# Performance work log

Hardware: AMD Instinct MI355X
Metric: run time of the kernel (lower is better)

The kernel has to match this reference:

```python
import jax, jax.numpy as jnp
import numpy as np
import math

EMBED = 768
HEADS = 12
DK = EMBED // HEADS
FFN = 3072
NQ = 8
B, S = 4, 2048


def _layernorm(x, g, b, eps=1e-5):
    mu = jnp.mean(x, axis=-1, keepdims=True)
    var = jnp.var(x, axis=-1, keepdims=True)
    return (x - mu) * jax.lax.rsqrt(var + eps) * g + b


def setup_inputs() -> dict:
    key = jax.random.key(0)
    ks = jax.random.split(key, 16)
    std = 0.02
    inp = {
        "x": jax.random.normal(ks[0], (B, S, EMBED), dtype=jnp.float32),
        "mask": jnp.ones((B, S), dtype=jnp.int32),
        # attention projections (torch Linear: W [out, in])
        "wq": jax.random.normal(ks[1], (EMBED, EMBED), jnp.float32) * std,
        "bq": jnp.zeros((EMBED,), jnp.float32),
        "wk": jax.random.normal(ks[2], (EMBED, EMBED), jnp.float32) * std,
        "bk": jnp.zeros((EMBED,), jnp.float32),
        "wv": jax.random.normal(ks[3], (EMBED, EMBED), jnp.float32) * std,
        "bv": jnp.zeros((EMBED,), jnp.float32),
        "wo": jax.random.normal(ks[4], (EMBED, EMBED), jnp.float32) * std,
        "bo": jnp.zeros((EMBED,), jnp.float32),
        # layernorms
        "g1": jnp.ones((EMBED,), jnp.float32),
        "be1": jnp.zeros((EMBED,), jnp.float32),
        "g2": jnp.ones((EMBED,), jnp.float32),
        "be2": jnp.zeros((EMBED,), jnp.float32),
        # quantum FFN: trainable RY angles + two linears
        "theta": jax.random.normal(ks[5], (NQ,), jnp.float32) * 0.1,
        "w1": jax.random.normal(ks[6], (FFN, NQ), jnp.float32) * std,
        "b1": jnp.zeros((FFN,), jnp.float32),
        "w2": jax.random.normal(ks[7], (EMBED, FFN), jnp.float32) * std,
        "b2": jnp.zeros((EMBED,), jnp.float32),
    }
    return inp


def _block(x, mask, wq, bq, wk, bk, wv, bv, wo, bo, g1, be1, g2, be2,
           theta, w1, b1, w2, b2):
    b, s, _ = x.shape
    # --- multi-head attention (dropout = identity at eval) ---
    q = (x @ wq.T + bq).reshape(b, s, HEADS, DK)
    k = (x @ wk.T + bk).reshape(b, s, HEADS, DK)
    v = (x @ wv.T + bv).reshape(b, s, HEADS, DK)
    scores = jnp.einsum("bqhd,bkhd->bhqk", q, k) / math.sqrt(DK)
    scores = jnp.where(mask[:, None, None, :] == 0, -1e9, scores)
    attn = jax.nn.softmax(scores, axis=-1)
    ctx = jnp.einsum("bhqk,bkhd->bqhd", attn, v).reshape(b, s, EMBED)
    attn_out = ctx @ wo.T + bo
    x = _layernorm(x + attn_out, g1, be1)
    # --- quantum FFN: RY(x_i) then RY(theta_i) on |0>, <Z> = cos(x_i+theta_i)
    # (product state, no entanglement -> exact closed form, fully batched)
    meas = jnp.cos(x[..., :NQ] + theta)            # [b, s, NQ]
    h = jax.nn.relu(meas @ w1.T + b1)              # [b, s, FFN]
    ffn_out = h @ w2.T + b2                        # [b, s, EMBED]
    return _layernorm(x + ffn_out, g2, be2)


def reference(x, mask, wq, bq, wk, bk, wv, bv, wo, bo, g1, be1, g2, be2,
              theta, w1, b1, w2, b2):
    return _block(x, mask, wq, bq, wk, bk, wv, bv, wo, bo,
                  g1, be1, g2, be2, theta, w1, b1, w2, b2)
```

## Files before the change

### kernel.cpp

```cpp
#include <hip/hip_runtime.h>
#include <hip/hip_bf16.h>


typedef __bf16 bf16_t;
typedef bf16_t bf16x4 __attribute__((ext_vector_type(4)));
typedef bf16_t bf16x8 __attribute__((ext_vector_type(8)));
typedef float floatx4 __attribute__((ext_vector_type(4)));

#define LOG2E 1.44269504088896f

__device__ __forceinline__ void gload16(const bf16_t* g, bf16_t* l) {
    __builtin_amdgcn_global_load_lds(
        (const __attribute__((address_space(1))) unsigned int*)g,
        (__attribute__((address_space(3))) unsigned int*)l,
        16, 0, 0);
}

__global__ __launch_bounds__(256)
void prep(const float* __restrict__ x,
          const float* __restrict__ wq, const float* __restrict__ wk,
          const float* __restrict__ wv, const float* __restrict__ wo,
          const float* __restrict__ w2,
          const float* __restrict__ bq, const float* __restrict__ bk,
          const float* __restrict__ bv,
          bf16_t* __restrict__ xb, bf16_t* __restrict__ wqkv,
          bf16_t* __restrict__ wob, bf16_t* __restrict__ w2b,
          float* __restrict__ bqkv)
{
    const int seg = blockIdx.y;
    const int idx = blockIdx.x * 256 + threadIdx.x;
    if (seg == 0) {
        if (idx >= 1572864) return;
        const float4 f = ((const float4*)x)[idx];
        bf16x4 o = {(bf16_t)f.x, (bf16_t)f.y, (bf16_t)f.z, (bf16_t)f.w};
        ((bf16x4*)xb)[idx] = o;
    } else if (seg == 1) {
        if (idx >= 442368) return;
        const int e = idx * 4;
        float4 f = (e < 589824) ? ((const float4*)wq)[idx]
                 : (e < 1179648) ? ((const float4*)wk)[idx - 147456]
                                 : ((const float4*)wv)[idx - 294912];
        if (e < 589824) { f.x *= 0.125f; f.y *= 0.125f; f.z *= 0.125f; f.w *= 0.125f; }
        bf16x4 o = {(bf16_t)f.x, (bf16_t)f.y, (bf16_t)f.z, (bf16_t)f.w};
        ((bf16x4*)wqkv)[idx] = o;
    } else if (seg == 2) {
        if (idx >= 147456) return;
        const float4 f = ((const float4*)wo)[idx];
        bf16x4 o = {(bf16_t)f.x, (bf16_t)f.y, (bf16_t)f.z, (bf16_t)f.w};
        ((bf16x4*)wob)[idx] = o;
    } else if (seg == 3) {
        if (idx >= 589824) return;
        const float4 f = ((const float4*)w2)[idx];
        bf16x4 o = {(bf16_t)f.x, (bf16_t)f.y, (bf16_t)f.z, (bf16_t)f.w};
        ((bf16x4*)w2b)[idx] = o;
    } else {
        if (idx >= 576) return;
        const int e = idx * 4;
        float4 f = (e < 768) ? ((const float4*)bq)[idx]
                 : (e < 1536) ? ((const float4*)bk)[idx - 192]
                              : ((const float4*)bv)[idx - 384];
        if (e < 768) { f.x *= 0.125f; f.y *= 0.125f; f.z *= 0.125f; f.w *= 0.125f; }
        ((float4*)bqkv)[idx] = f;
    }
}

template<typename TC>
__global__ __launch_bounds__(256)
void gemm_bb(const bf16_t* __restrict__ A, const bf16_t* __restrict__ W,
             const float* __restrict__ bias, TC* __restrict__ C,
             int kPer, int lda, int ldw, int ldc, int splitStride)
{
    __shared__ __align__(16) bf16_t As[2][4096];
    __shared__ __align__(16) bf16_t Bs[2][4096];
    const int tid  = threadIdx.x;
    const int wave = tid >> 6;
    const int lane = tid & 63;
    const int wm = (wave >> 1) * 64;
    const int wn = (wave & 1) * 64;

    const int nwg  = gridDim.x * gridDim.y;
    const int flat = blockIdx.y * gridDim.x + blockIdx.x;
    const int swz  = (flat & 7) * (nwg >> 3) + (flat >> 3);
    const int bm = (swz / gridDim.x) * 128;
    const int bn = (swz % gridDim.x) * 128;

    const int fr = lane & 15;
    const int fk = (lane >> 4) * 8;

    const int kBeg = blockIdx.z * kPer;
    const int kEnd = kBeg + kPer;
    C += (size_t)blockIdx.z * splitStride;

    const int srow = tid >> 2;
    const int scol = (tid & 3) * 8;

    floatx4 acc[4][4] = {};

    const bf16_t* gA = A + (size_t)(bm + srow) * lda + scol;
    const bf16_t* gB = W + (size_t)(bn + srow) * ldw + scol;

#define STAGE(buf, kk)                                              \
    {   const bf16_t* ga = gA + (kk);                               \
        const bf16_t* gb = gB + (kk);                               \
        gload16(ga,                    &As[buf][tid * 8]);          \
        gload16(ga + (size_t)64 * lda, &As[buf][tid * 8 + 2048]);   \
        gload16(gb,                    &Bs[buf][tid * 8]);          \
        gload16(gb + (size_t)64 * ldw, &Bs[buf][tid * 8 + 2048]);   \
    }

    STAGE(0, kBeg);
    __syncthreads();

    int cur = 0;
    for (int k0 = kBeg; k0 < kEnd; k0 += 32) {
        if (k0 + 32 < kEnd) STAGE(cur ^ 1, k0 + 32);

        bf16x8 fa[4], fb[4];
        #pragma unroll
        for (int i = 0; i < 4; ++i) {
            fa[i] = *(const bf16x8*)&As[cur][(wm + i * 16 + fr) * 32 + fk];
            fb[i] = *(const bf16x8*)&Bs[cur][(wn + i * 16 + fr) * 32 + fk];
        }
        #pragma unroll
        for (int mi = 0; mi < 4; ++mi)
            #pragma unroll
            for (int ni = 0; ni < 4; ++ni)
                acc[mi][ni] = __builtin_amdgcn_mfma_f32_16x16x32_bf16(
                    fa[mi], fb[ni], acc[mi][ni], 0, 0, 0);

        __syncthreads();
        cur ^= 1;
    }
#undef STAGE

    const int fg = (lane >> 4) * 4;
    const bool addb = (blockIdx.z == 0);
    #pragma unroll
    for (int mi = 0; mi < 4; ++mi) {
        #pragma unroll
        for (int ni = 0; ni < 4; ++ni) {
            const int col = bn + wn + ni * 16 + fr;
            const float bv = addb ? bias[col] : 0.f;
            #pragma unroll
            for (int r = 0; r < 4; ++r) {
                const int row = bm + wm + mi * 16 + fg + r;
                C[(size_t)row * ldc + col] = (TC)(acc[mi][ni][r] + bv);
            }
        }
    }
}

__global__ __launch_bounds__(256)
void attn_mfma(const bf16_t* __restrict__ qkv, const int* __restrict__ mask,
               bf16_t* __restrict__ ctx)
{
    __shared__ bf16_t Ks[64][72];
    __shared__ bf16_t Vt[80][72];
    __shared__ float  mb_s[64];
    __shared__ bf16_t Pl[4][32][72];

    const int flat = blockIdx.x;
    const int swz  = (flat & 7) * 96 + (flat >> 3);
    const int bh = swz >> 4;
    const int b = bh / 12, h = bh % 12;
    const int tid  = threadIdx.x;
    const int wave = tid >> 6;
    const int lane = tid & 63;
    const int g    = lane >> 4;
    const int fr   = lane & 15;
    const int qbase = (swz & 15) * 128 + wave * 32;

    for (int idx = tid; idx < 16 * 72; idx += 256) {
        const int rr = idx / 72, cc = idx % 72;
        Vt[64 + rr][cc] = (bf16_t)(rr == 0 ? 1.f : 0.f);
    }

    bf16x8 qf[2][2];
    #pragma unroll
    for (int qt = 0; qt < 2; ++qt)
        #pragma unroll
        for (int s = 0; s < 2; ++s) {
            const size_t tok = (size_t)(b * 2048 + qbase + qt * 16 + fr);
            qf[qt][s] = *(const bf16x8*)(qkv + tok * 2304 + h * 64 + s * 32 + g * 8);
        }

    floatx4 o[2][4] = {};
    floatx4 oe[2] = {};

    const int skey = tid & 63;
    const int sgrp = tid >> 6;

    bf16x8 rk0, rk1, rv0, rv1;
    float  rmb;
    {
        const size_t ktok = (size_t)(b * 2048 + skey) * 2304 + h * 64;
        rk0 = *(const bf16x8*)(qkv + ktok + 768 + sgrp * 16);
        rk1 = *(const bf16x8*)(qkv + ktok + 768 + sgrp * 16 + 8);
        rv0 = *(const bf16x8*)(qkv + ktok + 1536 + sgrp * 16);
        rv1 = *(const bf16x8*)(qkv + ktok + 1536 + sgrp * 16 + 8);
        rmb = (mask[b * 2048 + skey] == 0) ? -1e9f : 0.f;
    }

    for (int kt = 0; kt < 32; ++kt) {
        __syncthreads();
        *(bf16x8*)&Ks[skey][sgrp * 16]     = rk0;
        *(bf16x8*)&Ks[skey][sgrp * 16 + 8] = rk1;
        #pragma unroll
        for (int j = 0; j < 8; ++j) {
            Vt[sgrp * 16 + j][skey]     = rv0[j];
            Vt[sgrp * 16 + 8 + j][skey] = rv1[j];
        }
        if (tid < 64) mb_s[tid] = rmb;
        __syncthreads();

        if (kt + 1 < 32) {
            const size_t ktok = (size_t)(b * 2048 + (kt + 1) * 64 + skey) * 2304 + h * 64;
            rk0 = *(const bf16x8*)(qkv + ktok + 768 + sgrp * 16);
            rk1 = *(const bf16x8*)(qkv + ktok + 768 + sgrp * 16 + 8);
            rv0 = *(const bf16x8*)(qkv + ktok + 1536 + sgrp * 16);
            rv1 = *(const bf16x8*)(qkv + ktok + 1536 + sgrp * 16 + 8);
            rmb = (mask[b * 2048 + (kt + 1) * 64 + skey] == 0) ? -1e9f : 0.f;
        }

        floatx4 st_[2][4] = {};
        #pragma unroll
        for (int s = 0; s < 2; ++s) {
            bf16x8 kf[4];
            #pragma unroll
            for (int ct = 0; ct < 4; ++ct)
                kf[ct] = *(const bf16x8*)&Ks[ct * 16 + fr][s * 32 + g * 8];
            #pragma unroll
            for (int qt = 0; qt < 2; ++qt)
                #pragma unroll
                for (int ct = 0; ct < 4; ++ct)
                    st_[qt][ct] = __builtin_amdgcn_mfma_f32_16x16x32_bf16(
                        kf[ct], qf[qt][s], st_[qt][ct], 0, 0, 0);
        }

        #pragma unroll
        for (int qt = 0; qt < 2; ++qt) {
            #pragma unroll
            for (int ct = 0; ct < 4; ++ct) {
                const float4 mb4 = *(const float4*)&mb_s[ct * 16 + g * 4];
                const float mbr[4] = { mb4.x, mb4.y, mb4.z, mb4.w };
                bf16x4 pw;
                #pragma unroll
                for (int r = 0; r < 4; ++r)
                    pw[r] = (bf16_t)__builtin_amdgcn_exp2f(
                        fmaf(st_[qt][ct][r], LOG2E, mbr[r]));
                *(bf16x4*)&Pl[wave][qt * 16 + fr][ct * 16 + g * 4] = pw;
            }
        }

        #pragma unroll
        for (int st2 = 0; st2 < 2; ++st2) {
            bf16x8 pf[2];
            #pragma unroll
            for (int qt = 0; qt < 2; ++qt)
                pf[qt] = *(const bf16x8*)&Pl[wave][qt * 16 + fr][st2 * 32 + g * 8];
            #pragma unroll
            for (int dt = 0; dt < 4; ++dt) {
                const bf16x8 vf = *(const bf16x8*)&Vt[dt * 16 + fr][st2 * 32 + g * 8];
                #pragma unroll
                for (int qt = 0; qt < 2; ++qt)
                    o[qt][dt] = __builtin_amdgcn_mfma_f32_16x16x32_bf16(
                        pf[qt], vf, o[qt][dt], 0, 0, 0);
            }
            const bf16x8 vo = *(const bf16x8*)&Vt[64 + fr][st2 * 32 + g * 8];
            #pragma unroll
            for (int qt = 0; qt < 2; ++qt)
                oe[qt] = __builtin_amdgcn_mfma_f32_16x16x32_bf16(
                    pf[qt], vo, oe[qt], 0, 0, 0);
        }
    }

    #pragma unroll
    for (int qt = 0; qt < 2; ++qt) {
        float inv[4];
        #pragma unroll
        for (int r = 0; r < 4; ++r) {
            const float lv = __shfl(oe[qt][r], (lane & 48), 64);
            inv[r] = 1.f / lv;
        }
        #pragma unroll
        for (int dt = 0; dt < 4; ++dt)
            #pragma unroll
            for (int r = 0; r < 4; ++r) {
                const size_t row = (size_t)(b * 2048 + qbase + qt * 16 + g * 4 + r);
                ctx[row * 768 + h * 64 + dt * 16 + fr] = (bf16_t)(o[qt][dt][r] * inv[r]);
            }
    }
}

__global__ __launch_bounds__(256)
void ln_fuse(const float* __restrict__ xin, const float* __restrict__ proj,
             const float* __restrict__ proj2,
             const float* __restrict__ g, const float* __restrict__ be,
             float* __restrict__ out,
             const float* __restrict__ theta, float* __restrict__ meas)
{
    const int wave = threadIdx.x >> 6;
    const int lane = threadIdx.x & 63;
    const int row  = blockIdx.x * 4 + wave;
    const size_t base = (size_t)row * 768;

    float4 v[3];
    float s1 = 0.f, s2 = 0.f;
    #pragma unroll
    for (int i = 0; i < 3; ++i) {
        const int c4 = lane + i * 64;
        const float4 a  = ((const float4*)(xin  + base))[c4];
        const float4 p  = ((const float4*)(proj + base))[c4];
        const float4 p2 = ((const float4*)(proj2 + base))[c4];
        v[i].x = a.x + p.x + p2.x;
        v[i].y = a.y + p.y + p2.y;
        v[i].z = a.z + p.z + p2.z;
        v[i].w = a.w + p.w + p2.w;
        s1 += v[i].x + v[i].y + v[i].z + v[i].w;
        s2 += v[i].x*v[i].x + v[i].y*v[i].y + v[i].z*v[i].z + v[i].w*v[i].w;
    }
    #pragma unroll
    for (int mk = 32; mk >= 1; mk >>= 1) {
        s1 += __shfl_xor(s1, mk, 64);
        s2 += __shfl_xor(s2, mk, 64);
    }
    const float mu   = s1 * (1.f / 768.f);
    const float var  = s2 * (1.f / 768.f) - mu * mu;
    const float rinv = rsqrtf(var + 1e-5f);

    #pragma unroll
    for (int i = 0; i < 3; ++i) {
        const int c4 = lane + i * 64;
        const float4 gg = ((const float4*)g)[c4];
        const float4 bb = ((const float4*)be)[c4];
        float4 o;
        o.x = (v[i].x - mu) * rinv * gg.x + bb.x;
        o.y = (v[i].y - mu) * rinv * gg.y + bb.y;
        o.z = (v[i].z - mu) * rinv * gg.z + bb.z;
        o.w = (v[i].w - mu) * rinv * gg.w + bb.w;
        ((float4*)(out + base))[c4] = o;
        if (i == 0 && meas != nullptr && lane < 2) {
            meas[row * 8 + lane * 4 + 0] = cosf(o.x + theta[lane * 4 + 0]);
            meas[row * 8 + lane * 4 + 1] = cosf(o.y + theta[lane * 4 + 1]);
            meas[row * 8 + lane * 4 + 2] = cosf(o.z + theta[lane * 4 + 2]);
            meas[row * 8 + lane * 4 + 3] = cosf(o.w + theta[lane * 4 + 3]);
        }
    }
}

__global__ __launch_bounds__(256)
void ffn1(const float* __restrict__ meas, const float* __restrict__ w1,
          const float* __restrict__ b1, bf16_t* __restrict__ h)
{
    const int row = blockIdx.x;
    __shared__ float ms[8];
    if (threadIdx.x < 8) ms[threadIdx.x] = meas[row * 8 + threadIdx.x];
    __syncthreads();
    #pragma unroll
    for (int i = 0; i < 12; ++i) {
        const int f = threadIdx.x + i * 256;
        const float4 wa = *(const float4*)(w1 + f * 8);
        const float4 wb = *(const float4*)(w1 + f * 8 + 4);
        float v = b1[f];
        v += ms[0]*wa.x + ms[1]*wa.y + ms[2]*wa.z + ms[3]*wa.w;
        v += ms[4]*wb.x + ms[5]*wb.y + ms[6]*wb.z + ms[7]*wb.w;
        h[(size_t)row * 3072 + f] = (bf16_t)fmaxf(v, 0.f);
    }
}

extern "C" void kernel_launch(void* const* d_in, const int* in_sizes, int n_in,
                              void* d_out, int out_size, void* d_ws, size_t ws_size,
                              hipStream_t stream)
{
    const float* x     = (const float*)d_in[0];
    const int*   mask  = (const int*)d_in[1];
    const float* wq    = (const float*)d_in[2];
    const float* bq    = (const float*)d_in[3];
    const float* wk    = (const float*)d_in[4];
    const float* bk    = (const float*)d_in[5];
    const float* wv    = (const float*)d_in[6];
    const float* bv    = (const float*)d_in[7];
    const float* wo    = (const float*)d_in[8];
    const float* bo    = (const float*)d_in[9];
    const float* g1    = (const float*)d_in[10];
    const float* be1   = (const float*)d_in[11];
    const float* g2    = (const float*)d_in[12];
    const float* be2   = (const float*)d_in[13];
    const float* theta = (const float*)d_in[14];
    const float* w1    = (const float*)d_in[15];
    const float* b1    = (const float*)d_in[16];
    const float* w2    = (const float*)d_in[17];
    const float* b2    = (const float*)d_in[18];
    float* out = (float*)d_out;

    char* ws = (char*)d_ws;
    bf16_t* qkv    = (bf16_t*)(ws + 0);
    bf16_t* ctx    = (bf16_t*)(ws + 37748736);
    float*  attnp  = (float*)(ws + 50331648);
    float*  y      = (float*)(ws + 100663296);
    float*  meas   = (float*)(ws + 125829120);
    bf16_t* xb     = (bf16_t*)(ws + 126091264);
    bf16_t* wqkv   = (bf16_t*)(ws + 138674176);
    bf16_t* wob    = (bf16_t*)(ws + 142213120);
    bf16_t* w2b    = (bf16_t*)(ws + 143392768);
    float*  bqkv   = (float*)(ws + 148111360);
    float*  ffnp   = (float*)(ws + 0);
    bf16_t* h      = (bf16_t*)(ws + 50331648);

    const dim3 blk(256);

    prep<<<dim3(6144, 5), blk, 0, stream>>>(x, wq, wk, wv, wo, w2, bq, bk, bv,
                                            xb, wqkv, wob, w2b, bqkv);

    gemm_bb<bf16_t><<<dim3(18, 64, 1), blk, 0, stream>>>(
        xb, wqkv, bqkv, qkv, 768, 768, 768, 2304, 0);

    attn_mfma<<<dim3(768), blk, 0, stream>>>(qkv, mask, ctx);

    gemm_bb<float><<<dim3(6, 64, 2), blk, 0, stream>>>(
        ctx, wob, bo, attnp, 384, 768, 768, 768, 6291456);

    ln_fuse<<<dim3(2048), blk, 0, stream>>>(x, attnp, attnp + 6291456,
                                            g1, be1, y, theta, meas);

    ffn1<<<dim3(8192), blk, 0, stream>>>(meas, w1, b1, h);

    gemm_bb<float><<<dim3(6, 64, 2), blk, 0, stream>>>(
        h, w2b, b2, ffnp, 1536, 3072, 3072, 768, 6291456);

    ln_fuse<<<dim3(2048), blk, 0, stream>>>(y, ffnp, ffnp + 6291456,
                                            g2, be2, out, nullptr, nullptr);
}
```

Measured before the change: 293.0 us.

## Double-buffer attention LDS tiles, XOR-swizzle layout, compute row sums in registers

The attention kernel now keeps two LDS buffers for the K, transposed-V and mask tiles. This cuts the per-iteration barriers from two to one, so the next tile can be stored while the current one is consumed. The padded LDS arrays become XOR-swizzled 64-column layouts to avoid bank conflicts without padding. The softmax denominator is now summed in fp32 registers and reduced with lane shuffles, replacing the extra MFMA against a ones column. In exchange, LDS use roughly doubles for K and V, and the indexing needs a few more integer ops.

```diff
diff --git a/kernel.cpp b/kernel.cpp
--- a/kernel.cpp
+++ b/kernel.cpp
@@ -14,6 +14,10 @@
         (const __attribute__((address_space(1))) unsigned int*)g,
         (__attribute__((address_space(3))) unsigned int*)l,
         16, 0, 0);
+}
+
+__device__ __forceinline__ int swz(int row, int col) {
+    return row * 64 + (col ^ ((row & 7) << 3));
 }
 
 __global__ __launch_bounds__(256)
@@ -80,9 +84,9 @@
 
     const int nwg  = gridDim.x * gridDim.y;
     const int flat = blockIdx.y * gridDim.x + blockIdx.x;
-    const int swz  = (flat & 7) * (nwg >> 3) + (flat >> 3);
-    const int bm = (swz / gridDim.x) * 128;
-    const int bn = (swz % gridDim.x) * 128;
+    const int swzb = (flat & 7) * (nwg >> 3) + (flat >> 3);
+    const int bm = (swzb / gridDim.x) * 128;
+    const int bn = (swzb % gridDim.x) * 128;
 
     const int fr = lane & 15;
     const int fk = (lane >> 4) * 8;
@@ -154,26 +158,21 @@
 void attn_mfma(const bf16_t* __restrict__ qkv, const int* __restrict__ mask,
                bf16_t* __restrict__ ctx)
 {
-    __shared__ bf16_t Ks[64][72];
-    __shared__ bf16_t Vt[80][72];
-    __shared__ float  mb_s[64];
-    __shared__ bf16_t Pl[4][32][72];
+    __shared__ __align__(16) bf16_t KsL[2][4096];
+    __shared__ __align__(16) bf16_t VtL[2][4096];
+    __shared__ __align__(16) bf16_t PlL[4][2048];
+    __shared__ float mbL[2][64];
 
     const int flat = blockIdx.x;
-    const int swz  = (flat & 7) * 96 + (flat >> 3);
-    const int bh = swz >> 4;
+    const int swzb = (flat & 7) * 96 + (flat >> 3);
+    const int bh = swzb >> 4;
     const int b = bh / 12, h = bh % 12;
     const int tid  = threadIdx.x;
     const int wave = tid >> 6;
     const int lane = tid & 63;
     const int g    = lane >> 4;
     const int fr   = lane & 15;
-    const int qbase = (swz & 15) * 128 + wave * 32;
-
-    for (int idx = tid; idx < 16 * 72; idx += 256) {
-        const int rr = idx / 72, cc = idx % 72;
-        Vt[64 + rr][cc] = (bf16_t)(rr == 0 ? 1.f : 0.f);
-    }
+    const int qbase = (swzb & 15) * 128 + wave * 32;
 
     bf16x8 qf[2][2];
     #pragma unroll
@@ -185,7 +184,7 @@
         }
 
     floatx4 o[2][4] = {};
-    floatx4 oe[2] = {};
+    float lsum[2] = {0.f, 0.f};
 
     const int skey = tid & 63;
     const int sgrp = tid >> 6;
@@ -201,17 +200,16 @@
         rmb = (mask[b * 2048 + skey] == 0) ? -1e9f : 0.f;
     }
 
+    int cur = 0;
     for (int kt = 0; kt < 32; ++kt) {
-        __syncthreads();
-        *(bf16x8*)&Ks[skey][sgrp * 16]     = rk0;
-        *(bf16x8*)&Ks[skey][sgrp * 16 + 8] = rk1;
+        *(bf16x8*)&KsL[cur][swz(skey, sgrp * 16)]     = rk0;
+        *(bf16x8*)&KsL[cur][swz(skey, sgrp * 16 + 8)] = rk1;
         #pragma unroll
         for (int j = 0; j < 8; ++j) {
-            Vt[sgrp * 16 + j][skey]     = rv0[j];
-            Vt[sgrp * 16 + 8 + j][skey] = rv1[j];
-        }
-        if (tid < 64) mb_s[tid] = rmb;
-        __syncthreads();
+            VtL[cur][swz(sgrp * 16 + j,     skey)] = rv0[j];
+            VtL[cur][swz(sgrp * 16 + 8 + j, skey)] = rv1[j];
+        }
+        if (tid < 64) mbL[cur][tid] = rmb;
 
         if (kt + 1 < 32) {
             const size_t ktok = (size_t)(b * 2048 + (kt + 1) * 64 + skey) * 2304 + h * 64;
@@ -222,13 +220,15 @@
             rmb = (mask[b * 2048 + (kt + 1) * 64 + skey] == 0) ? -1e9f : 0.f;
         }
 
+        __syncthreads();
+
         floatx4 st_[2][4] = {};
         #pragma unroll
         for (int s = 0; s < 2; ++s) {
             bf16x8 kf[4];
             #pragma unroll
             for (int ct = 0; ct < 4; ++ct)
-                kf[ct] = *(const bf16x8*)&Ks[ct * 16 + fr][s * 32 + g * 8];
+                kf[ct] = *(const bf16x8*)&KsL[cur][swz(ct * 16 + fr, s * 32 + g * 8)];
             #pragma unroll
             for (int qt = 0; qt < 2; ++qt)
                 #pragma unroll
@@ -241,14 +241,17 @@
         for (int qt = 0; qt < 2; ++qt) {
             #pragma unroll
             for (int ct = 0; ct < 4; ++ct) {
-                const float4 mb4 = *(const float4*)&mb_s[ct * 16 + g * 4];
+                const float4 mb4 = *(const float4*)&mbL[cur][ct * 16 + g * 4];
                 const float mbr[4] = { mb4.x, mb4.y, mb4.z, mb4.w };
                 bf16x4 pw;
                 #pragma unroll
-                for (int r = 0; r < 4; ++r)
-                    pw[r] = (bf16_t)__builtin_amdgcn_exp2f(
+                for (int r = 0; r < 4; ++r) {
+                    const float p = __builtin_amdgcn_exp2f(
                         fmaf(st_[qt][ct][r], LOG2E, mbr[r]));
-                *(bf16x4*)&Pl[wave][qt * 16 + fr][ct * 16 + g * 4] = pw;
+                    lsum[qt] += p;
+                    pw[r] = (bf16_t)p;
+                }
+                *(bf16x4*)&PlL[wave][swz(qt * 16 + fr, ct * 16 + g * 4)] = pw;
             }
         }
 
@@ -257,29 +260,29 @@
             bf16x8 pf[2];
             #pragma unroll
             for (int qt = 0; qt < 2; ++qt)
-                pf[qt] = *(const bf16x8*)&Pl[wave][qt * 16 + fr][st2 * 32 + g * 8];
+                pf[qt] = *(const bf16x8*)&PlL[wave][swz(qt * 16 + fr, st2 * 32 + g * 8)];
             #pragma unroll
             for (int dt = 0; dt < 4; ++dt) {
-                const bf16x8 vf = *(const bf16x8*)&Vt[dt * 16 + fr][st2 * 32 + g * 8];
+                const bf16x8 vf = *(const bf16x8*)&VtL[cur][swz(dt * 16 + fr, st2 * 32 + g * 8)];
                 #pragma unroll
                 for (int qt = 0; qt < 2; ++qt)
                     o[qt][dt] = __builtin_amdgcn_mfma_f32_16x16x32_bf16(
                         pf[qt], vf, o[qt][dt], 0, 0, 0);
             }
-            const bf16x8 vo = *(const bf16x8*)&Vt[64 + fr][st2 * 32 + g * 8];
-            #pragma unroll
-            for (int qt = 0; qt < 2; ++qt)
-                oe[qt] = __builtin_amdgcn_mfma_f32_16x16x32_bf16(
-                    pf[qt], vo, oe[qt], 0, 0, 0);
-        }
+        }
+
+        cur ^= 1;
     }
 
     #pragma unroll
     for (int qt = 0; qt < 2; ++qt) {
+        float lf = lsum[qt];
+        lf += __shfl_xor(lf, 16, 64);
+        lf += __shfl_xor(lf, 32, 64);
         float inv[4];
         #pragma unroll
         for (int r = 0; r < 4; ++r) {
-            const float lv = __shfl(oe[qt][r], (lane & 48), 64);
+            const float lv = __shfl(lf, (lane & 48) + g * 4 + r, 64);
             inv[r] = 1.f / lv;
         }
         #pragma unroll
```

Result: no change. 295.7 us (+0.9%).
